# Performance work log

Hardware: AMD Instinct MI355X
Metric: run time of the kernel (lower is better)

The kernel has to match this reference:

```python
import jax, jax.numpy as jnp
import numpy as np

D_MODEL = 512
D_STATE = 64
BATCH = 8
SEQ_L = 4096


def setup_inputs() -> dict:
    key = jax.random.key(0)
    k_u, k_c, k_d = jax.random.split(key, 3)
    u = jax.random.normal(k_u, (BATCH, D_MODEL, SEQ_L), dtype=jnp.float32)
    # B buffer: zeros with first state column = 1 (fixed shift-SSM input matrix)
    B = jnp.zeros((D_MODEL, D_STATE), dtype=jnp.float32).at[:, 0].set(1.0)
    C = jax.random.normal(k_c, (1, D_MODEL, D_STATE), dtype=jnp.float32)
    D = jax.random.normal(k_d, (D_MODEL,), dtype=jnp.float32)
    return {"u": u, "B": B, "C": C, "D": D}


def reference(u, B, C, D):
    """Shift state-space layer. u: (batch, H, L) -> (batch, H, L)."""
    L = u.shape[-1]
    n = 2 * L  # pad to 2L so circular conv == linear (causal) conv
    B_fc = jnp.conj(jnp.fft.rfft(B, n=n))            # (H, n//2+1)
    C_f = jnp.fft.rfft(C, n=n)                       # (1, H, n//2+1)
    kernel = jnp.fft.irfft(B_fc * C_f, n=n)[..., :L]  # (1, H, L)
    kernel_f = jnp.fft.rfft(kernel, n=n)             # (1, H, n//2+1)
    u_f = jnp.fft.rfft(u, n=n)                       # (batch, H, n//2+1)
    y = jnp.fft.irfft(u_f * kernel_f, n=n)[..., :L]  # (batch, H, L)
    return y + u * D[:, None]
```

## Files before the change

### kernel.cpp

```cpp
#include <hip/hip_runtime.h>
#include <hip/hip_bf16.h>


#define D_MODEL 512
#define D_STATE 64
#define BATCH   8
#define SEQ_L   4096
#define NT      256

typedef short           s16x8 __attribute__((ext_vector_type(8)));
typedef unsigned short  u16;
typedef u16             u16x4 __attribute__((ext_vector_type(4)));
typedef u16             u16x8 __attribute__((ext_vector_type(8)));
typedef float           f32x4 __attribute__((ext_vector_type(4)));

__device__ __forceinline__ int SW(int g) { return g ^ ((g >> 3) & 7); }

__device__ __forceinline__ u16 f2bf(float f) {
    unsigned v = __builtin_bit_cast(unsigned, f);
    return (u16)((v + 0x7FFFu + ((v >> 16) & 1u)) >> 16);
}

__global__ void __launch_bounds__(NT)
shift_mfma(const float* __restrict__ u, const float* __restrict__ B,
           const float* __restrict__ C, const float* __restrict__ D,
           float* __restrict__ y) {
    const int row = blockIdx.x;
    const int h   = row & (D_MODEL - 1);
    const float* __restrict__ urow = u + (size_t)row * SEQ_L;
    float* __restrict__ yrow       = y + (size_t)row * SEQ_L;

    __shared__ u16   ub[536 * 8];
    __shared__ float Bs[64];
    __shared__ float Cs[128];
    __shared__ float Kf[64];

    const int t = threadIdx.x;

    if (t < 16) {
        ((float4*)Bs)[t] = ((const float4*)(B + h * D_STATE))[t];
    } else if (t < 48) {
        const int j = t - 16;
        ((float4*)Cs)[j] = (j < 16) ? ((const float4*)(C + h * D_STATE))[j]
                                    : make_float4(0.f, 0.f, 0.f, 0.f);
    }

    #pragma unroll
    for (int j = 0; j < 4; ++j) {
        const float4 v = *(const float4*)(urow + 4 * t + 1024 * j);
        u16x4 pk = { f2bf(v.x), f2bf(v.y), f2bf(v.z), f2bf(v.w) };
        const int byte = 128 + 8 * t + 2048 * j;
        const int sb   = (SW(byte >> 4) << 4) | (byte & 8);
        *(u16x4*)((char*)ub + sb) = pk;
    }
    if (t < 8) {
        u16x8 z = {0,0,0,0,0,0,0,0};
        *(u16x8*)((char*)ub + (SW(t) << 4)) = z;
    } else if (t < 20) {
        u16x8 z = {0,0,0,0,0,0,0,0};
        const int g = 520 + (t - 8);
        *(u16x8*)((char*)ub + (SW(g) << 4)) = z;
    }
    __syncthreads();

    if (t < D_STATE) {
        float s = 0.f;
        #pragma unroll
        for (int j = 0; j < D_STATE; ++j) s = fmaf(Bs[j], Cs[t + j], s);
        if (t == 0) s += D[h];
        Kf[t] = s;
    }
    __syncthreads();

    const int l = t & 63;
    const int n = l & 15;
    const int q = l >> 4;
    s16x8 bfr[3];
    #pragma unroll
    for (int c = 0; c < 3; ++c) {
        #pragma unroll
        for (int j = 0; j < 8; ++j) {
            const int p = 32 * c + 8 * q + j;
            const int k = 64 + n - p;
            const float v = (k >= 0 && k < D_STATE) ? Kf[k] : 0.f;
            bfr[c][j] = (short)f2bf(v);
        }
    }

    const int wbase = 1024 * (t >> 6);
    #pragma unroll
    for (int tt = 0; tt < 4; ++tt) {
        const int base = wbase + 256 * tt;
        f32x4 acc = {0.f, 0.f, 0.f, 0.f};
        #pragma unroll
        for (int c = 0; c < 3; ++c) {
            const int L  = base + 16 * n + 32 * c + 8 * q;
            const int sb = SW(L >> 3) << 4;
            const s16x8 a = *(const s16x8*)((const char*)ub + sb);
            acc = __builtin_amdgcn_mfma_f32_16x16x32_bf16(a, bfr[c], acc, 0, 0, 0);
        }
        #pragma unroll
        for (int r = 0; r < 4; ++r)
            yrow[base + 16 * (4 * q + r) + n] = acc[r];
    }
}

extern "C" void kernel_launch(void* const* d_in, const int* in_sizes, int n_in,
                              void* d_out, int out_size, void* d_ws, size_t ws_size,
                              hipStream_t stream) {
    const float* u = (const float*)d_in[0];
    const float* B = (const float*)d_in[1];
    const float* C = (const float*)d_in[2];
    const float* D = (const float*)d_in[3];
    float* y = (float*)d_out;

    shift_mfma<<<dim3(BATCH * D_MODEL), dim3(NT), 0, stream>>>(u, B, C, D, y);
}
```

Before: 120.4 us.

## Precompute per-channel taps and MFMA B fragments in a separate kernel

Splits the tap computation (B·C correlation plus D) into a small prologue kernel that writes the taps and pre-packed bf16 MFMA B fragments to workspace, so each of the 4096 main blocks no longer recomputes them for its channel. The main kernel loads fragments directly and issues the u loads before the LDS writes to overlap latency, and one __syncthreads is removed. In exchange it adds a second kernel launch and extra global reads of fragments, and falls back to building fragments from global taps if the workspace is too small.

```diff
diff --git a/kernel.cpp b/kernel.cpp
--- a/kernel.cpp
+++ b/kernel.cpp
@@ -14,6 +14,9 @@
 typedef u16             u16x8 __attribute__((ext_vector_type(8)));
 typedef float           f32x4 __attribute__((ext_vector_type(4)));
 
+#define K_BYTES    (D_MODEL * D_STATE * 4)
+#define FRAG_BYTES (D_MODEL * 3 * 64 * 16)
+
 __device__ __forceinline__ int SW(int g) { return g ^ ((g >> 3) & 7); }
 
 __device__ __forceinline__ u16 f2bf(float f) {
@@ -21,21 +24,15 @@
     return (u16)((v + 0x7FFFu + ((v >> 16) & 1u)) >> 16);
 }
 
-__global__ void __launch_bounds__(NT)
-shift_mfma(const float* __restrict__ u, const float* __restrict__ B,
-           const float* __restrict__ C, const float* __restrict__ D,
-           float* __restrict__ y) {
-    const int row = blockIdx.x;
-    const int h   = row & (D_MODEL - 1);
-    const float* __restrict__ urow = u + (size_t)row * SEQ_L;
-    float* __restrict__ yrow       = y + (size_t)row * SEQ_L;
-
-    __shared__ u16   ub[536 * 8];
-    __shared__ float Bs[64];
-    __shared__ float Cs[128];
-    __shared__ float Kf[64];
-
+__global__ void __launch_bounds__(64)
+taps_kernel(const float* __restrict__ B, const float* __restrict__ C,
+            const float* __restrict__ D, float* __restrict__ Kws,
+            u16x8* __restrict__ F, int do_frags) {
+    const int h = blockIdx.x;
     const int t = threadIdx.x;
+    __shared__ float Bs[D_STATE];
+    __shared__ float Cs[2 * D_STATE];
+    __shared__ float Kf[D_STATE];
 
     if (t < 16) {
         ((float4*)Bs)[t] = ((const float4*)(B + h * D_STATE))[t];
@@ -44,48 +41,83 @@
         ((float4*)Cs)[j] = (j < 16) ? ((const float4*)(C + h * D_STATE))[j]
                                     : make_float4(0.f, 0.f, 0.f, 0.f);
     }
+    __syncthreads();
 
+    float s = 0.f;
     #pragma unroll
-    for (int j = 0; j < 4; ++j) {
-        const float4 v = *(const float4*)(urow + 4 * t + 1024 * j);
-        u16x4 pk = { f2bf(v.x), f2bf(v.y), f2bf(v.z), f2bf(v.w) };
-        const int byte = 128 + 8 * t + 2048 * j;
-        const int sb   = (SW(byte >> 4) << 4) | (byte & 8);
-        *(u16x4*)((char*)ub + sb) = pk;
+    for (int j = 0; j < D_STATE; ++j) s = fmaf(Bs[j], Cs[t + j], s);
+    if (t == 0) s += D[h];
+    Kws[h * D_STATE + t] = s;
+    Kf[t] = s;
+    __syncthreads();
+
+    if (do_frags) {
+        const int n = t & 15, q = t >> 4;
+        #pragma unroll
+        for (int c = 0; c < 3; ++c) {
+            u16x8 fr;
+            #pragma unroll
+            for (int j = 0; j < 8; ++j) {
+                const int k = 64 + n - (32 * c + 8 * q + j);
+                fr[j] = (k >= 0 && k < D_STATE) ? f2bf(Kf[k]) : (u16)0;
+            }
+            F[(h * 3 + c) * 64 + t] = fr;
+        }
     }
+}
+
+template <bool FRAGS>
+__global__ void __launch_bounds__(NT)
+shift_mfma(const float* __restrict__ u, const float* __restrict__ Kws,
+           const u16x8* __restrict__ F, float* __restrict__ y) {
+    const int row = blockIdx.x;
+    const int h   = row & (D_MODEL - 1);
+    const float* __restrict__ urow = u + (size_t)row * SEQ_L;
+    float* __restrict__ yrow       = y + (size_t)row * SEQ_L;
+
+    __shared__ u16 ub[536 * 8];
+
+    const int t = threadIdx.x;
+    const int l = t & 63, n = l & 15, q = l >> 4;
+
+    s16x8 bfr[3];
+    if (FRAGS) {
+        #pragma unroll
+        for (int c = 0; c < 3; ++c)
+            bfr[c] = __builtin_bit_cast(s16x8, F[(h * 3 + c) * 64 + l]);
+    }
+
+    float4 v[4];
+    #pragma unroll
+    for (int j = 0; j < 4; ++j)
+        v[j] = *(const float4*)(urow + 4 * t + 1024 * j);
+
     if (t < 8) {
         u16x8 z = {0,0,0,0,0,0,0,0};
         *(u16x8*)((char*)ub + (SW(t) << 4)) = z;
     } else if (t < 20) {
         u16x8 z = {0,0,0,0,0,0,0,0};
-        const int g = 520 + (t - 8);
-        *(u16x8*)((char*)ub + (SW(g) << 4)) = z;
+        *(u16x8*)((char*)ub + (SW(520 + t - 8) << 4)) = z;
+    }
+    #pragma unroll
+    for (int j = 0; j < 4; ++j) {
+        u16x4 pk = { f2bf(v[j].x), f2bf(v[j].y), f2bf(v[j].z), f2bf(v[j].w) };
+        const int byte = 128 + 8 * t + 2048 * j;
+        const int sb   = (SW(byte >> 4) << 4) | (byte & 8);
+        *(u16x4*)((char*)ub + sb) = pk;
+    }
+
+    if (!FRAGS) {
+        const float* Kg = Kws + h * D_STATE;
+        #pragma unroll
+        for (int c = 0; c < 3; ++c)
+            #pragma unroll
+            for (int j = 0; j < 8; ++j) {
+                const int k = 64 + n - (32 * c + 8 * q + j);
+                bfr[c][j] = (short)((k >= 0 && k < D_STATE) ? f2bf(Kg[k]) : (u16)0);
+            }
     }
     __syncthreads();
-
-    if (t < D_STATE) {
-        float s = 0.f;
-        #pragma unroll
-        for (int j = 0; j < D_STATE; ++j) s = fmaf(Bs[j], Cs[t + j], s);
-        if (t == 0) s += D[h];
-        Kf[t] = s;
-    }
-    __syncthreads();
-
-    const int l = t & 63;
-    const int n = l & 15;
-    const int q = l >> 4;
-    s16x8 bfr[3];
-    #pragma unroll
-    for (int c = 0; c < 3; ++c) {
-        #pragma unroll
-        for (int j = 0; j < 8; ++j) {
-            const int p = 32 * c + 8 * q + j;
-            const int k = 64 + n - p;
-            const float v = (k >= 0 && k < D_STATE) ? Kf[k] : 0.f;
-            bfr[c][j] = (short)f2bf(v);
-        }
-    }
 
     const int wbase = 1024 * (t >> 6);
     #pragma unroll
@@ -114,5 +146,14 @@
     const float* D = (const float*)d_in[3];
     float* y = (float*)d_out;
 
-    shift_mfma<<<dim3(BATCH * D_MODEL), dim3(NT), 0, stream>>>(u, B, C, D, y);
+    float* Kws = (float*)d_ws;
+    u16x8* F   = (u16x8*)((char*)d_ws + K_BYTES);
+    const bool frags = ws_size >= (size_t)(K_BYTES + FRAG_BYTES);
+
+    taps_kernel<<<dim3(D_MODEL), dim3(64), 0, stream>>>(B, C, D, Kws, F,
+                                                        frags ? 1 : 0);
+    if (frags)
+        shift_mfma<true><<<dim3(BATCH * D_MODEL), dim3(NT), 0, stream>>>(u, Kws, F, y);
+    else
+        shift_mfma<false><<<dim3(BATCH * D_MODEL), dim3(NT), 0, stream>>>(u, Kws, F, y);
 }
```

Result: no change. 121.2 us (+0.6%).
